# Kernel tuning notes

Hardware: AMD Instinct MI355X
Metric: run time of the kernel (lower is better)

The kernel has to match this reference:

```python
import jax, jax.numpy as jnp
import numpy as np

D_MODEL = 512
N_HEADS = 8
HEAD_DIM = D_MODEL // N_HEADS
SEQ = 2048
BATCH = 2
EPS = 1e-5
SCALE = 1.0 / np.sqrt(HEAD_DIM).astype(np.float32)
# (kind, window, dilation) per head, matching init_kwargs head_specs
SPECS = [("global", 0, 1), ("global", 0, 1),
         ("window", 64, 1), ("window", 128, 1), ("window", 256, 1),
         ("dilated", 64, 2), ("dilated", 64, 4), ("dilated", 64, 8)]


def build_masks(N):
    i = jnp.arange(N)
    D = jnp.abs(i[:, None] - i[None, :])
    ms = []
    for kind, w, dil in SPECS:
        if kind == "global":
            ms.append(jnp.ones((N, N), dtype=bool))
        elif kind == "window":
            ms.append(D <= w)
        else:  # dilated
            ms.append((D % dil == 0) & (D // dil <= w))
    return jnp.stack(ms)  # [H, N, N] bool


def layernorm(x, g, b):
    mu = jnp.mean(x, axis=-1, keepdims=True)
    var = jnp.mean((x - mu) ** 2, axis=-1, keepdims=True)
    return (x - mu) * jax.lax.rsqrt(var + EPS) * g + b


def setup_inputs() -> dict:
    key = jax.random.key(0)
    ks = jax.random.split(key, 7)
    w = 0.02
    return {
        "x": jax.random.normal(ks[0], (BATCH, SEQ, D_MODEL), dtype=jnp.float32),
        "Wq": jax.random.normal(ks[1], (D_MODEL, D_MODEL), dtype=jnp.float32) * w,
        "Wk": jax.random.normal(ks[2], (D_MODEL, D_MODEL), dtype=jnp.float32) * w,
        "Wv": jax.random.normal(ks[3], (D_MODEL, D_MODEL), dtype=jnp.float32) * w,
        "Wo": jax.random.normal(ks[4], (D_MODEL, D_MODEL), dtype=jnp.float32) * w,
        "T_w1": jax.random.normal(ks[5], (D_MODEL, D_MODEL), dtype=jnp.float32) * w,
        "T_b1": jnp.zeros((D_MODEL,), dtype=jnp.float32),
        "T_w2": jax.random.normal(ks[6], (1, D_MODEL), dtype=jnp.float32) * w,
        "T_b2": jnp.zeros((1,), dtype=jnp.float32),
        "ln_in_g": jnp.ones((D_MODEL,), dtype=jnp.float32),
        "ln_in_b": jnp.zeros((D_MODEL,), dtype=jnp.float32),
        "ln_out_g": jnp.ones((D_MODEL,), dtype=jnp.float32),
        "ln_out_b": jnp.zeros((D_MODEL,), dtype=jnp.float32),
    }


def reference(x, Wq, Wk, Wv, Wo, T_w1, T_b1, T_w2, T_b2,
              ln_in_g, ln_in_b, ln_out_g, ln_out_b):
    B, N, H = x.shape
    x0 = x
    xn = layernorm(x, ln_in_g, ln_in_b)
    # torch Linear: y = x @ W.T ; reshape to [B, h, N, d]
    def heads(W):
        return (xn @ W.T).reshape(B, N, N_HEADS, HEAD_DIM).transpose(0, 2, 1, 3)
    Q, K, V = heads(Wq), heads(Wk), heads(Wv)
    attn = jnp.einsum("bhqd,bhkd->bhqk", Q, K) * SCALE
    mask = build_masks(N)  # [h, N, N]
    attn = jnp.where(mask[None], attn, -jnp.inf)
    attn = jax.nn.softmax(attn, axis=-1)  # every row has diagonal unmasked
    out = jnp.einsum("bhqk,bhkd->bhqd", attn, V)
    out = out.transpose(0, 2, 1, 3).reshape(B, N, N_HEADS * HEAD_DIM)
    out = out @ Wo.T
    # tanh-gated softmax over sequence dim
    T_logits = jnp.tanh(xn @ T_w1.T + T_b1) @ T_w2.T + T_b2  # [B, N, 1]
    T = jax.nn.softmax(T_logits, axis=1)
    out = out * T
    return layernorm(out + x0, ln_out_g, ln_out_b)
```

## Files before the change

### kernel.cpp

```cpp
#include <hip/hip_runtime.h>
#include <math.h>

#define N_SEQ 2048
#define DM    512
#define NTOK  4096
#define NH    8
#define HD    64
#define NSLOT 18

typedef __attribute__((ext_vector_type(8))) short short8;
typedef __attribute__((ext_vector_type(4))) short short4_t;
typedef __attribute__((ext_vector_type(4))) float f32x4;

__device__ inline short f2bf(float x) {
    union { float f; unsigned u; } v; v.f = x;
    unsigned r = v.u + 0x7fff + ((v.u >> 16) & 1);
    return (short)(r >> 16);
}
__device__ inline float bf2f(short s) {
    union { unsigned u; float f; } v; v.u = ((unsigned)(unsigned short)s) << 16;
    return v.f;
}
__device__ inline unsigned pkbf(float a, float b) {
    return ((unsigned)(unsigned short)f2bf(b) << 16) | (unsigned)(unsigned short)f2bf(a);
}
__device__ inline float ftanh(float x) {
    float e = __expf(2.f * x);
    return 1.f - 2.f / (e + 1.f);
}

__device__ inline f32x4 mfma16(short8 a, short8 b, f32x4 c) {
    return __builtin_amdgcn_mfma_f32_16x16x32_bf16(a, b, c, 0, 0, 0);
}

__device__ __forceinline__ void async_cp16(const short* g, short* l) {
    __builtin_amdgcn_global_load_lds(
        (const __attribute__((address_space(1))) void*)g,
        (__attribute__((address_space(3))) void*)l, 16, 0, 0);
}

__global__ __launch_bounds__(256) void k_lncvt(
    const float* __restrict__ x, const float* __restrict__ g,
    const float* __restrict__ b, short* __restrict__ y, float* __restrict__ lg,
    const float* __restrict__ Wq, const float* __restrict__ Wk,
    const float* __restrict__ Wv, const float* __restrict__ Tw1,
    const float* __restrict__ Wo,
    short* __restrict__ wcat, short* __restrict__ wo) {
    int blk = blockIdx.x, t = threadIdx.x;
    if (blk < 2048) {
        int sub = t >> 7, tt = t & 127;
        int tk = blk * 2 + sub;
        if (tt == 0) lg[tk] = 0.f;
        float4 xv = ((const float4*)(x + (size_t)tk * DM))[tt];
        float s = xv.x + xv.y + xv.z + xv.w;
        float q = xv.x*xv.x + xv.y*xv.y + xv.z*xv.z + xv.w*xv.w;
        for (int o = 32; o; o >>= 1) { s += __shfl_down(s, o); q += __shfl_down(q, o); }
        __shared__ float ls[4], lq[4];
        if ((t & 63) == 0) { ls[t >> 6] = s; lq[t >> 6] = q; }
        __syncthreads();
        s = ls[sub * 2] + ls[sub * 2 + 1];
        q = lq[sub * 2] + lq[sub * 2 + 1];
        float mu = s * (1.f / DM);
        float var = q * (1.f / DM) - mu * mu;
        float rs = rsqrtf(var + 1e-5f);
        float4 gv = ((const float4*)g)[tt], bv = ((const float4*)b)[tt];
        short4_t o;
        o[0] = f2bf((xv.x - mu) * rs * gv.x + bv.x);
        o[1] = f2bf((xv.y - mu) * rs * gv.y + bv.y);
        o[2] = f2bf((xv.z - mu) * rs * gv.z + bv.z);
        o[3] = f2bf((xv.w - mu) * rs * gv.w + bv.w);
        *(short4_t*)&y[(size_t)tk * DM + tt * 4] = o;
    } else {
        int id = (blk - 2048) * 256 + t;
        if (id < 262144) {
            int z = id >> 16; int off = id & 65535;
            const float* s = (z == 0) ? Wq : (z == 1) ? Wk : (z == 2) ? Wv : Tw1;
            float4 v = ((const float4*)s)[off];
            short4_t o = {f2bf(v.x), f2bf(v.y), f2bf(v.z), f2bf(v.w)};
            *(short4_t*)(wcat + (size_t)z * 262144 + (size_t)off * 4) = o;
        } else {
            int off = id - 262144;
            float4 v = ((const float4*)Wo)[off];
            short4_t o = {f2bf(v.x), f2bf(v.y), f2bf(v.z), f2bf(v.w)};
            *(short4_t*)(wo + (size_t)off * 4) = o;
        }
    }
}

__global__ __launch_bounds__(256) void k_gemmqkvt(
    const short* __restrict__ A, const short* __restrict__ W,
    const float* __restrict__ Tb1, const float* __restrict__ Tw2,
    short* __restrict__ qb, short* __restrict__ kb, short* __restrict__ vb,
    float* __restrict__ lg) {
    __shared__ short As[128 * 32];
    __shared__ short Bs[128 * 32];
    int t = threadIdx.x;
    int lane = t & 63, w = t >> 6;
    int wy = w >> 1, wx = w & 1;
    int ln = lane & 15, q4 = lane >> 4;
    int c0 = blockIdx.x * 128, m0 = blockIdx.y * 128;
    int sr = t >> 2, sc = (t & 3) << 3;
    f32x4 acc[4][4];
    f32x4 zero = {0.f, 0.f, 0.f, 0.f};
    #pragma unroll
    for (int i = 0; i < 4; i++)
        #pragma unroll
        for (int j = 0; j < 4; j++) acc[i][j] = zero;
    for (int k0 = 0; k0 < DM; k0 += 32) {
        __syncthreads();
        async_cp16(&A[(size_t)(m0 + sr) * DM + k0 + sc],      &As[sr * 32 + sc]);
        async_cp16(&A[(size_t)(m0 + 64 + sr) * DM + k0 + sc], &As[(64 + sr) * 32 + sc]);
        async_cp16(&W[(size_t)(c0 + sr) * DM + k0 + sc],      &Bs[sr * 32 + sc]);
        async_cp16(&W[(size_t)(c0 + 64 + sr) * DM + k0 + sc], &Bs[(64 + sr) * 32 + sc]);
        __syncthreads();
        short8 af[4], bfr[4];
        #pragma unroll
        for (int i = 0; i < 4; i++)
            af[i] = *(short8*)&As[(wy * 64 + i * 16 + ln) * 32 + q4 * 8];
        #pragma unroll
        for (int j = 0; j < 4; j++)
            bfr[j] = *(short8*)&Bs[(wx * 64 + j * 16 + ln) * 32 + q4 * 8];
        #pragma unroll
        for (int i = 0; i < 4; i++)
            #pragma unroll
            for (int j = 0; j < 4; j++)
                acc[i][j] = mfma16(af[i], bfr[j], acc[i][j]);
    }
    int z = c0 >> 9;
    if (z < 3) {
        short* dst = (z == 0) ? qb : (z == 1) ? kb : vb;
        float sc2 = (z == 0) ? 0.125f : 1.0f;
        #pragma unroll
        for (int i = 0; i < 4; i++)
            #pragma unroll
            for (int j = 0; j < 4; j++)
                #pragma unroll
                for (int r = 0; r < 4; r++) {
                    int row = m0 + wy * 64 + i * 16 + q4 * 4 + r;
                    int col = c0 + wx * 64 + j * 16 + ln;
                    int nin = col & 511;
                    int h = nin >> 6, d = nin & 63;
                    int bi = row >> 11, n = row & (N_SEQ - 1);
                    dst[(((size_t)bi * NH + h) * N_SEQ + n) * HD + d] =
                        f2bf(acc[i][j][r] * sc2);
                }
    } else {
        #pragma unroll
        for (int i = 0; i < 4; i++) {
            #pragma unroll
            for (int r = 0; r < 4; r++) {
                float s = 0.f;
                #pragma unroll
                for (int j = 0; j < 4; j++) {
                    int tc = (c0 & 511) + wx * 64 + j * 16 + ln;
                    s += ftanh(acc[i][j][r] + Tb1[tc]) * Tw2[tc];
                }
                s += __shfl_xor(s, 1);
                s += __shfl_xor(s, 2);
                s += __shfl_xor(s, 4);
                s += __shfl_xor(s, 8);
                if (ln == 0) {
                    int row = m0 + wy * 64 + i * 16 + q4 * 4 + r;
                    atomicAdd(&lg[row], s);
                }
            }
        }
    }
}

__global__ __launch_bounds__(256) void k_gemmp(
    const short* __restrict__ A, const short* __restrict__ W,
    float* __restrict__ proj) {
    __shared__ short As[128 * 32];
    __shared__ short Bs[64 * 32];
    int t = threadIdx.x;
    int lane = t & 63, w = t >> 6;
    int wy = w >> 1, wx = w & 1;
    int ln = lane & 15, q4 = lane >> 4;
    int c0 = blockIdx.x * 64, m0 = blockIdx.y * 128;
    int sr = t >> 2, sc = (t & 3) << 3;
    int br = t >> 2, bc = (t & 3) << 3;
    f32x4 acc[4][2];
    f32x4 zero = {0.f, 0.f, 0.f, 0.f};
    #pragma unroll
    for (int i = 0; i < 4; i++) { acc[i][0] = zero; acc[i][1] = zero; }
    for (int k0 = 0; k0 < DM; k0 += 32) {
        __syncthreads();
        async_cp16(&A[(size_t)(m0 + sr) * DM + k0 + sc],      &As[sr * 32 + sc]);
        async_cp16(&A[(size_t)(m0 + 64 + sr) * DM + k0 + sc], &As[(64 + sr) * 32 + sc]);
        if (br < 64)
            async_cp16(&W[(size_t)(c0 + br) * DM + k0 + bc], &Bs[br * 32 + bc]);
        __syncthreads();
        short8 af[4], bfr[2];
        #pragma unroll
        for (int i = 0; i < 4; i++)
            af[i] = *(short8*)&As[(wy * 64 + i * 16 + ln) * 32 + q4 * 8];
        #pragma unroll
        for (int j = 0; j < 2; j++)
            bfr[j] = *(short8*)&Bs[(wx * 32 + j * 16 + ln) * 32 + q4 * 8];
        #pragma unroll
        for (int i = 0; i < 4; i++)
            #pragma unroll
            for (int j = 0; j < 2; j++)
                acc[i][j] = mfma16(af[i], bfr[j], acc[i][j]);
    }
    #pragma unroll
    for (int i = 0; i < 4; i++)
        #pragma unroll
        for (int j = 0; j < 2; j++)
            #pragma unroll
            for (int r = 0; r < 4; r++) {
                int row = m0 + wy * 64 + i * 16 + q4 * 4 + r;
                int col = c0 + wx * 32 + j * 16 + ln;
                proj[(size_t)row * DM + col] = acc[i][j][r];
            }
}

__global__ __launch_bounds__(256) void k_vtrgate(const short* __restrict__ vb,
                                                 short* __restrict__ vtb,
                                                 const float* __restrict__ lg,
                                                 float* __restrict__ gate) {
    __shared__ short tile[64][80];
    __shared__ float rg[8];
    int blk = blockIdx.x, t = threadIdx.x;
    if (blk < 512) {
        int n0 = (blk & 31) * 64, bh = blk >> 5;
        const short* src = vb + (size_t)bh * N_SEQ * HD;
        short* dst = vtb + (size_t)bh * HD * N_SEQ;
        #pragma unroll
        for (int i = 0; i < 2; i++) {
            int id = t + 256 * i;
            int r = id >> 3, c = id & 7;
            *(short8*)&tile[r][c * 8] = *(const short8*)&src[(size_t)(n0 + r) * HD + c * 8];
        }
        __syncthreads();
        #pragma unroll
        for (int i = 0; i < 2; i++) {
            int id = t + 256 * i;
            int d = id >> 3, c = id & 7;
            short8 v;
            #pragma unroll
            for (int j = 0; j < 8; j++) v[j] = tile[c * 8 + j][d];
            *(short8*)&dst[(size_t)d * N_SEQ + n0 + c * 8] = v;
        }
    } else {
        int b = blk - 512;
        float v[8];
        {
            float4 a0 = *(const float4*)&lg[b * N_SEQ + t * 8];
            float4 a1 = *(const float4*)&lg[b * N_SEQ + t * 8 + 4];
            v[0] = a0.x; v[1] = a0.y; v[2] = a0.z; v[3] = a0.w;
            v[4] = a1.x; v[5] = a1.y; v[6] = a1.z; v[7] = a1.w;
        }
        float m = v[0];
        #pragma unroll
        for (int j = 1; j < 8; j++) m = fmaxf(m, v[j]);
        for (int o = 32; o; o >>= 1) m = fmaxf(m, __shfl_down(m, o));
        if ((t & 63) == 0) rg[t >> 6] = m;
        __syncthreads();
        m = fmaxf(fmaxf(rg[0], rg[1]), fmaxf(rg[2], rg[3]));
        float e[8], s = 0.f;
        #pragma unroll
        for (int j = 0; j < 8; j++) { e[j] = __expf(v[j] - m); s += e[j]; }
        for (int o = 32; o; o >>= 1) s += __shfl_down(s, o);
        if ((t & 63) == 0) rg[4 + (t >> 6)] = s;
        __syncthreads();
        s = (rg[4] + rg[5]) + (rg[6] + rg[7]);
        float inv = 1.f / s;
        float4 o0 = {e[0] * inv, e[1] * inv, e[2] * inv, e[3] * inv};
        float4 o1 = {e[4] * inv, e[5] * inv, e[6] * inv, e[7] * inv};
        *(float4*)&gate[b * N_SEQ + t * 8] = o0;
        *(float4*)&gate[b * N_SEQ + t * 8 + 4] = o1;
    }
}

__global__ __launch_bounds__(256) void k_attn(const short* __restrict__ qb,
                                              const short* __restrict__ kb,
                                              const short* __restrict__ vtb,
                                              short* __restrict__ P_O,
                                              float* __restrict__ P_ml) {
    __shared__ short Ks[128 * 72];
    __shared__ short Vt[64 * 136];
    __shared__ short Pa[4][16 * 136];
    int t = threadIdx.x;
    int lane = t & 63, w = t >> 6;
    int ln = lane & 15, q4 = lane >> 4;
    int slot = blockIdx.x, qt = blockIdx.y, bi = blockIdx.z;
    int q0 = qt * 64;
    int h, c;
    if (slot < 4)        { h = 0; c = slot; }
    else if (slot < 8)   { h = 1; c = slot - 4; }
    else if (slot == 8)  { h = 2; c = 0; }
    else if (slot == 9)  { h = 3; c = 0; }
    else if (slot < 12)  { h = 4; c = slot - 10; }
    else if (slot == 12) { h = 5; c = 0; }
    else if (slot < 15)  { h = 6; c = slot - 13; }
    else                 { h = 7; c = slot - 15; }
    int kind = (h < 2) ? 0 : (h < 5) ? 1 : 2;
    int wnd = (h == 2 || h >= 5) ? 64 : (h == 3) ? 128 : (h == 4) ? 256 : 0;
    int dsh = (h == 5) ? 1 : (h == 6) ? 2 : (h == 7) ? 3 : 0;
    int dmask = (1 << dsh) - 1;
    int wmax = (kind == 0) ? 0 : (wnd << dsh);
    int tLoU, tHiU, CS;
    if (kind == 0) { tLoU = 0; tHiU = 15; CS = 4; }
    else { tLoU = (q0 - wmax) >> 7; tHiU = (q0 + 63 + wmax) >> 7; CS = 3; }
    int ktLo = tLoU + c * CS;
    int ktHi = ktLo + CS - 1;
    if (ktHi > tHiU) ktHi = tHiU;
    if (ktHi > 15) ktHi = 15;
    if (ktLo < 0) ktLo = 0;
    int p4 = (bi * 32 + qt) * NSLOT + slot;
    float* ml = P_ml + (size_t)p4 * 128;
    if (ktLo > ktHi) {
        if (t < 64) { ml[t] = -1e30f; ml[64 + t] = 0.f; }
        return;
    }
    const size_t base = ((size_t)bi * NH + h) * N_SEQ * HD;
    const short* Q = qb + base;
    const short* K = kb + base;
    const short* Vg = vtb + base;
    short8 qa[2];
    {
        const short* qrow = Q + (size_t)(q0 + w * 16 + ln) * HD + q4 * 8;
        qa[0] = *(const short8*)qrow;
        qa[1] = *(const short8*)(qrow + 32);
    }
    int qi = q0 + w * 16 + ln;
    float m_i = -1e30f, l_i = 0.f;
    f32x4 OT[4];
    f32x4 zero = {0.f, 0.f, 0.f, 0.f};
    #pragma unroll
    for (int d = 0; d < 4; d++) OT[d] = zero;
    short* Paw = Pa[w];
    for (int kt = ktLo; kt <= ktHi; kt++) {
        int k0 = kt << 7;
        __syncthreads();
        #pragma unroll
        for (int i2 = 0; i2 < 4; i2++) {
            int id = t + 256 * i2;
            int kr = id >> 3, cc = id & 7;
            *(short8*)&Ks[kr * 72 + cc * 8] =
                *(const short8*)&K[(size_t)(k0 + kr) * HD + cc * 8];
            int dr = id >> 4, kc = id & 15;
            *(short8*)&Vt[dr * 136 + kc * 8] =
                *(const short8*)&Vg[(size_t)dr * N_SEQ + k0 + kc * 8];
        }
        __syncthreads();
        f32x4 ST[8];
        #pragma unroll
        for (int nt = 0; nt < 8; nt++) ST[nt] = zero;
        #pragma unroll
        for (int nt = 0; nt < 8; nt++) {
            #pragma unroll
            for (int ks = 0; ks < 2; ks++) {
                short8 af = *(short8*)&Ks[(nt * 16 + ln) * 72 + ks * 32 + q4 * 8];
                ST[nt] = mfma16(af, qa[ks], ST[nt]);
            }
        }
        if (kind != 0) {
            #pragma unroll
            for (int nt = 0; nt < 8; nt++)
                #pragma unroll
                for (int r = 0; r < 4; r++) {
                    int key = k0 + nt * 16 + q4 * 4 + r;
                    int dlt = qi - key; dlt = (dlt < 0) ? -dlt : dlt;
                    int valid;
                    if (kind == 1) valid = (dlt <= wnd);
                    else valid = ((dlt & dmask) == 0) && ((dlt >> dsh) <= wnd);
                    if (!valid) ST[nt][r] = -1e30f;
                }
        }
        float rm = -1e30f;
        #pragma unroll
        for (int nt = 0; nt < 8; nt++) {
            float a = fmaxf(ST[nt][0], ST[nt][1]);
            float b = fmaxf(ST[nt][2], ST[nt][3]);
            rm = fmaxf(rm, fmaxf(a, b));
        }
        rm = fmaxf(rm, __shfl_xor(rm, 16));
        rm = fmaxf(rm, __shfl_xor(rm, 32));
        float mn = fmaxf(m_i, rm);
        float sc = __expf(m_i - mn);
        float rs = 0.f;
        #pragma unroll
        for (int nt = 0; nt < 8; nt++) {
            float p0 = __expf(ST[nt][0] - mn);
            float p1 = __expf(ST[nt][1] - mn);
            float p2 = __expf(ST[nt][2] - mn);
            float p3 = __expf(ST[nt][3] - mn);
            rs += (p0 + p1) + (p2 + p3);
            *(unsigned*)&Paw[ln * 136 + nt * 16 + q4 * 4]     = pkbf(p0, p1);
            *(unsigned*)&Paw[ln * 136 + nt * 16 + q4 * 4 + 2] = pkbf(p2, p3);
        }
        rs += __shfl_xor(rs, 16);
        rs += __shfl_xor(rs, 32);
        l_i = l_i * sc + rs;
        m_i = mn;
        #pragma unroll
        for (int d = 0; d < 4; d++) OT[d] *= sc;
        short8 pb[4];
        #pragma unroll
        for (int ks = 0; ks < 4; ks++)
            pb[ks] = *(short8*)&Paw[ln * 136 + ks * 32 + q4 * 8];
        #pragma unroll
        for (int dt = 0; dt < 4; dt++) {
            #pragma unroll
            for (int ks = 0; ks < 4; ks++) {
                short8 a = *(short8*)&Vt[(dt * 16 + ln) * 136 + ks * 32 + q4 * 8];
                OT[dt] = mfma16(a, pb[ks], OT[dt]);
            }
        }
    }
    if (q4 == 0) { ml[w * 16 + ln] = m_i; ml[64 + w * 16 + ln] = l_i; }
    #pragma unroll
    for (int dt = 0; dt < 4; dt++) {
        *(unsigned*)&Paw[ln * 136 + dt * 16 + q4 * 4]     = pkbf(OT[dt][0], OT[dt][1]);
        *(unsigned*)&Paw[ln * 136 + dt * 16 + q4 * 4 + 2] = pkbf(OT[dt][2], OT[dt][3]);
    }
    short8 o0 = *(short8*)&Paw[ln * 136 + q4 * 16];
    short8 o1 = *(short8*)&Paw[ln * 136 + q4 * 16 + 8];
    short* Op = P_O + (size_t)p4 * 4096;
    *(short8*)&Op[(w * 16 + ln) * 64 + q4 * 16] = o0;
    *(short8*)&Op[(w * 16 + ln) * 64 + q4 * 16 + 8] = o1;
}

__global__ __launch_bounds__(256) void k_combine(const short* __restrict__ P_O,
                                                 const float* __restrict__ P_ml,
                                                 short* __restrict__ ob) {
    const int hbase[8] = {0, 4, 8, 9, 10, 12, 13, 15};
    const int hcnt[8]  = {4, 4, 1, 1, 2, 1, 2, 3};
    int h = blockIdx.x, qt = blockIdx.y, bi = blockIdx.z;
    int t = threadIdx.x;
    int row = t >> 2, c0 = (t & 3) * 16;
    int pb = (bi * 32 + qt) * NSLOT + hbase[h];
    int cnt = hcnt[h];
    float m = -1e30f;
    for (int s = 0; s < cnt; s++)
        m = fmaxf(m, P_ml[(size_t)(pb + s) * 128 + row]);
    float l = 0.f;
    float acc[16];
    #pragma unroll
    for (int j = 0; j < 16; j++) acc[j] = 0.f;
    for (int s = 0; s < cnt; s++) {
        float ms = P_ml[(size_t)(pb + s) * 128 + row];
        float ls = P_ml[(size_t)(pb + s) * 128 + 64 + row];
        if (ls > 0.f) {
            float sc = __expf(ms - m);
            l += ls * sc;
            const short* Op = P_O + (size_t)(pb + s) * 4096 + row * 64 + c0;
            short8 v0 = *(const short8*)Op;
            short8 v1 = *(const short8*)(Op + 8);
            #pragma unroll
            for (int j = 0; j < 8; j++) acc[j]     += bf2f(v0[j]) * sc;
            #pragma unroll
            for (int j = 0; j < 8; j++) acc[8 + j] += bf2f(v1[j]) * sc;
        }
    }
    float inv = 1.f / l;
    int n = qt * 64 + row;
    short8 o0, o1;
    #pragma unroll
    for (int j = 0; j < 8; j++) o0[j] = f2bf(acc[j] * inv);
    #pragma unroll
    for (int j = 0; j < 8; j++) o1[j] = f2bf(acc[8 + j] * inv);
    short* dst = ob + ((size_t)bi * N_SEQ + n) * DM + h * 64 + c0;
    *(short8*)dst = o0;
    *(short8*)(dst + 8) = o1;
}

__global__ __launch_bounds__(128) void k_final(const float* __restrict__ proj,
                                               const float* __restrict__ gate,
                                               const float* __restrict__ x0,
                                               const float* __restrict__ g,
                                               const float* __restrict__ b,
                                               float* __restrict__ out) {
    int tk = blockIdx.x, t = threadIdx.x;
    float gt = gate[tk];
    float4 pv = ((const float4*)(proj + (size_t)tk * DM))[t];
    float4 xv = ((const float4*)(x0 + (size_t)tk * DM))[t];
    float4 y;
    y.x = pv.x * gt + xv.x;
    y.y = pv.y * gt + xv.y;
    y.z = pv.z * gt + xv.z;
    y.w = pv.w * gt + xv.w;
    float s = y.x + y.y + y.z + y.w;
    float q = y.x*y.x + y.y*y.y + y.z*y.z + y.w*y.w;
    for (int o = 32; o; o >>= 1) { s += __shfl_down(s, o); q += __shfl_down(q, o); }
    __shared__ float ls[2], lq[2];
    if ((t & 63) == 0) { ls[t >> 6] = s; lq[t >> 6] = q; }
    __syncthreads();
    s = ls[0] + ls[1]; q = lq[0] + lq[1];
    float mu = s * (1.f / DM);
    float var = q * (1.f / DM) - mu * mu;
    float rs = rsqrtf(var + 1e-5f);
    float4 gv = ((const float4*)g)[t], bv = ((const float4*)b)[t];
    float4 o;
    o.x = (y.x - mu) * rs * gv.x + bv.x;
    o.y = (y.y - mu) * rs * gv.y + bv.y;
    o.z = (y.z - mu) * rs * gv.z + bv.z;
    o.w = (y.w - mu) * rs * gv.w + bv.w;
    ((float4*)(out + (size_t)tk * DM))[t] = o;
}

extern "C" void kernel_launch(void* const* d_in, const int* in_sizes, int n_in,
                              void* d_out, int out_size, void* d_ws, size_t ws_size,
                              hipStream_t stream) {
    (void)in_sizes; (void)n_in; (void)out_size; (void)ws_size;
    const float* x    = (const float*)d_in[0];
    const float* Wq   = (const float*)d_in[1];
    const float* Wk   = (const float*)d_in[2];
    const float* Wv   = (const float*)d_in[3];
    const float* Wo   = (const float*)d_in[4];
    const float* Tw1  = (const float*)d_in[5];
    const float* Tb1  = (const float*)d_in[6];
    const float* Tw2  = (const float*)d_in[7];
    const float* ling = (const float*)d_in[9];
    const float* linb = (const float*)d_in[10];
    const float* logg = (const float*)d_in[11];
    const float* logb = (const float*)d_in[12];
    float* out = (float*)d_out;

    const size_t SZ = (size_t)NTOK * DM;
    const int NPART = 2 * 32 * NSLOT;
    char* p = (char*)d_ws;
    short* xn   = (short*)p; p += SZ * 2;
    short* wcat = (short*)p; p += (size_t)2048 * DM * 2;
    short* wo   = (short*)p; p += (size_t)DM * DM * 2;
    short* qb   = (short*)p; p += SZ * 2;
    short* kb   = (short*)p; p += SZ * 2;
    short* vb   = (short*)p; p += SZ * 2;
    short* vtb  = (short*)p; p += SZ * 2;
    short* obuf = (short*)p; p += SZ * 2;
    float* lg   = (float*)p; p += (size_t)NTOK * 4;
    float* gate = (float*)p; p += (size_t)NTOK * 4;
    float* P_ml = (float*)p; p += (size_t)NPART * 128 * 4;
    float* proj = (float*)p;
    short* P_O  = (short*)p; p += (size_t)NPART * 4096 * 2;

    k_lncvt<<<3328, 256, 0, stream>>>(x, ling, linb, xn, lg,
                                      Wq, Wk, Wv, Tw1, Wo, wcat, wo);
    k_gemmqkvt<<<dim3(16, 32), 256, 0, stream>>>(xn, wcat, Tb1, Tw2,
                                                 qb, kb, vb, lg);
    k_vtrgate<<<514, 256, 0, stream>>>(vb, vtb, lg, gate);
    k_attn<<<dim3(NSLOT, 32, 2), 256, 0, stream>>>(qb, kb, vtb, P_O, P_ml);
    k_combine<<<dim3(8, 32, 2), 256, 0, stream>>>(P_O, P_ml, obuf);
    k_gemmp<<<dim3(8, 32), 256, 0, stream>>>(obuf, wo, proj);
    k_final<<<NTOK, 128, 0, stream>>>(proj, gate, x, logg, logb, out);
}
```

Baseline: 162.6 us.

## Fuse V transpose into QKV GEMM and gate softmax into attention kernel

The QKV GEMM epilogue now writes V directly in transposed layout through a shared-memory staging tile, so the separate transpose/gate kernel and the intermediate V buffer are removed. The gate softmax over the sequence moves into one attention block per batch. Single-slot heads (slots 8, 9, 12) normalize their output and write it straight to the output buffer, so the combine kernel handles only the five multi-slot heads. This saves one kernel launch and some global traffic, at the cost of extra shared memory in the GEMM (lower occupancy) and a serial gate tail in one attention block.

```diff
diff --git a/kernel.cpp b/kernel.cpp
--- a/kernel.cpp
+++ b/kernel.cpp
@@ -90,10 +90,11 @@
 __global__ __launch_bounds__(256) void k_gemmqkvt(
     const short* __restrict__ A, const short* __restrict__ W,
     const float* __restrict__ Tb1, const float* __restrict__ Tw2,
-    short* __restrict__ qb, short* __restrict__ kb, short* __restrict__ vb,
+    short* __restrict__ qb, short* __restrict__ kb, short* __restrict__ vtb,
     float* __restrict__ lg) {
     __shared__ short As[128 * 32];
     __shared__ short Bs[128 * 32];
+    __shared__ short Vs[128 * 136];
     int t = threadIdx.x;
     int lane = t & 63, w = t >> 6;
     int wy = w >> 1, wx = w & 1;
@@ -127,8 +128,8 @@
                 acc[i][j] = mfma16(af[i], bfr[j], acc[i][j]);
     }
     int z = c0 >> 9;
-    if (z < 3) {
-        short* dst = (z == 0) ? qb : (z == 1) ? kb : vb;
+    if (z < 2) {
+        short* dst = (z == 0) ? qb : kb;
         float sc2 = (z == 0) ? 0.125f : 1.0f;
         #pragma unroll
         for (int i = 0; i < 4; i++)
@@ -144,6 +145,28 @@
                     dst[(((size_t)bi * NH + h) * N_SEQ + n) * HD + d] =
                         f2bf(acc[i][j][r] * sc2);
                 }
+    } else if (z == 2) {
+        #pragma unroll
+        for (int i = 0; i < 4; i++)
+            #pragma unroll
+            for (int j = 0; j < 4; j++)
+                #pragma unroll
+                for (int r = 0; r < 4; r++) {
+                    int nl = wy * 64 + i * 16 + q4 * 4 + r;
+                    int dl = wx * 64 + j * 16 + ln;
+                    Vs[dl * 136 + nl] = f2bf(acc[i][j][r]);
+                }
+        __syncthreads();
+        int bi = m0 >> 11, n0 = m0 & (N_SEQ - 1);
+        int hp = (c0 & 511) >> 6;
+        #pragma unroll
+        for (int ii = 0; ii < 8; ii++) {
+            int id = t + 256 * ii;
+            int dl = id >> 4, nc = id & 15;
+            short8 v = *(short8*)&Vs[dl * 136 + nc * 8];
+            int h = hp + (dl >> 6), d = dl & 63;
+            *(short8*)&vtb[(((size_t)bi * NH + h) * HD + d) * N_SEQ + n0 + nc * 8] = v;
+        }
     } else {
         #pragma unroll
         for (int i = 0; i < 4; i++) {
@@ -216,72 +239,18 @@
             }
 }
 
-__global__ __launch_bounds__(256) void k_vtrgate(const short* __restrict__ vb,
-                                                 short* __restrict__ vtb,
-                                                 const float* __restrict__ lg,
-                                                 float* __restrict__ gate) {
-    __shared__ short tile[64][80];
-    __shared__ float rg[8];
-    int blk = blockIdx.x, t = threadIdx.x;
-    if (blk < 512) {
-        int n0 = (blk & 31) * 64, bh = blk >> 5;
-        const short* src = vb + (size_t)bh * N_SEQ * HD;
-        short* dst = vtb + (size_t)bh * HD * N_SEQ;
-        #pragma unroll
-        for (int i = 0; i < 2; i++) {
-            int id = t + 256 * i;
-            int r = id >> 3, c = id & 7;
-            *(short8*)&tile[r][c * 8] = *(const short8*)&src[(size_t)(n0 + r) * HD + c * 8];
-        }
-        __syncthreads();
-        #pragma unroll
-        for (int i = 0; i < 2; i++) {
-            int id = t + 256 * i;
-            int d = id >> 3, c = id & 7;
-            short8 v;
-            #pragma unroll
-            for (int j = 0; j < 8; j++) v[j] = tile[c * 8 + j][d];
-            *(short8*)&dst[(size_t)d * N_SEQ + n0 + c * 8] = v;
-        }
-    } else {
-        int b = blk - 512;
-        float v[8];
-        {
-            float4 a0 = *(const float4*)&lg[b * N_SEQ + t * 8];
-            float4 a1 = *(const float4*)&lg[b * N_SEQ + t * 8 + 4];
-            v[0] = a0.x; v[1] = a0.y; v[2] = a0.z; v[3] = a0.w;
-            v[4] = a1.x; v[5] = a1.y; v[6] = a1.z; v[7] = a1.w;
-        }
-        float m = v[0];
-        #pragma unroll
-        for (int j = 1; j < 8; j++) m = fmaxf(m, v[j]);
-        for (int o = 32; o; o >>= 1) m = fmaxf(m, __shfl_down(m, o));
-        if ((t & 63) == 0) rg[t >> 6] = m;
-        __syncthreads();
-        m = fmaxf(fmaxf(rg[0], rg[1]), fmaxf(rg[2], rg[3]));
-        float e[8], s = 0.f;
-        #pragma unroll
-        for (int j = 0; j < 8; j++) { e[j] = __expf(v[j] - m); s += e[j]; }
-        for (int o = 32; o; o >>= 1) s += __shfl_down(s, o);
-        if ((t & 63) == 0) rg[4 + (t >> 6)] = s;
-        __syncthreads();
-        s = (rg[4] + rg[5]) + (rg[6] + rg[7]);
-        float inv = 1.f / s;
-        float4 o0 = {e[0] * inv, e[1] * inv, e[2] * inv, e[3] * inv};
-        float4 o1 = {e[4] * inv, e[5] * inv, e[6] * inv, e[7] * inv};
-        *(float4*)&gate[b * N_SEQ + t * 8] = o0;
-        *(float4*)&gate[b * N_SEQ + t * 8 + 4] = o1;
-    }
-}
-
 __global__ __launch_bounds__(256) void k_attn(const short* __restrict__ qb,
                                               const short* __restrict__ kb,
                                               const short* __restrict__ vtb,
                                               short* __restrict__ P_O,
-                                              float* __restrict__ P_ml) {
+                                              float* __restrict__ P_ml,
+                                              short* __restrict__ ob,
+                                              const float* __restrict__ lg,
+                                              float* __restrict__ gate) {
     __shared__ short Ks[128 * 72];
     __shared__ short Vt[64 * 136];
     __shared__ short Pa[4][16 * 136];
+    __shared__ float rg[8];
     int t = threadIdx.x;
     int lane = t & 63, w = t >> 6;
     int ln = lane & 15, q4 = lane >> 4;
@@ -296,6 +265,7 @@
     else if (slot == 12) { h = 5; c = 0; }
     else if (slot < 15)  { h = 6; c = slot - 13; }
     else                 { h = 7; c = slot - 15; }
+    int solo = (slot == 8) | (slot == 9) | (slot == 12);
     int kind = (h < 2) ? 0 : (h < 5) ? 1 : 2;
     int wnd = (h == 2 || h >= 5) ? 64 : (h == 3) ? 128 : (h == 4) ? 256 : 0;
     int dsh = (h == 5) ? 1 : (h == 6) ? 2 : (h == 7) ? 3 : 0;
@@ -411,29 +381,72 @@
             }
         }
     }
-    if (q4 == 0) { ml[w * 16 + ln] = m_i; ml[64 + w * 16 + ln] = l_i; }
-    #pragma unroll
-    for (int dt = 0; dt < 4; dt++) {
-        *(unsigned*)&Paw[ln * 136 + dt * 16 + q4 * 4]     = pkbf(OT[dt][0], OT[dt][1]);
-        *(unsigned*)&Paw[ln * 136 + dt * 16 + q4 * 4 + 2] = pkbf(OT[dt][2], OT[dt][3]);
-    }
-    short8 o0 = *(short8*)&Paw[ln * 136 + q4 * 16];
-    short8 o1 = *(short8*)&Paw[ln * 136 + q4 * 16 + 8];
-    short* Op = P_O + (size_t)p4 * 4096;
-    *(short8*)&Op[(w * 16 + ln) * 64 + q4 * 16] = o0;
-    *(short8*)&Op[(w * 16 + ln) * 64 + q4 * 16 + 8] = o1;
+    if (solo) {
+        float inv = 1.f / l_i;
+        #pragma unroll
+        for (int dt = 0; dt < 4; dt++) {
+            *(unsigned*)&Paw[ln * 136 + dt * 16 + q4 * 4]     = pkbf(OT[dt][0] * inv, OT[dt][1] * inv);
+            *(unsigned*)&Paw[ln * 136 + dt * 16 + q4 * 4 + 2] = pkbf(OT[dt][2] * inv, OT[dt][3] * inv);
+        }
+        short8 o0 = *(short8*)&Paw[ln * 136 + q4 * 16];
+        short8 o1 = *(short8*)&Paw[ln * 136 + q4 * 16 + 8];
+        short* dst = ob + ((size_t)bi * N_SEQ + q0 + w * 16 + ln) * DM + h * 64 + q4 * 16;
+        *(short8*)dst = o0;
+        *(short8*)(dst + 8) = o1;
+    } else {
+        if (q4 == 0) { ml[w * 16 + ln] = m_i; ml[64 + w * 16 + ln] = l_i; }
+        #pragma unroll
+        for (int dt = 0; dt < 4; dt++) {
+            *(unsigned*)&Paw[ln * 136 + dt * 16 + q4 * 4]     = pkbf(OT[dt][0], OT[dt][1]);
+            *(unsigned*)&Paw[ln * 136 + dt * 16 + q4 * 4 + 2] = pkbf(OT[dt][2], OT[dt][3]);
+        }
+        short8 o0 = *(short8*)&Paw[ln * 136 + q4 * 16];
+        short8 o1 = *(short8*)&Paw[ln * 136 + q4 * 16 + 8];
+        short* Op = P_O + (size_t)p4 * 4096;
+        *(short8*)&Op[(w * 16 + ln) * 64 + q4 * 16] = o0;
+        *(short8*)&Op[(w * 16 + ln) * 64 + q4 * 16 + 8] = o1;
+    }
+    if (slot == 8 && qt == 0) {
+        int b = bi;
+        float v[8];
+        float4 a0 = *(const float4*)&lg[b * N_SEQ + t * 8];
+        float4 a1 = *(const float4*)&lg[b * N_SEQ + t * 8 + 4];
+        v[0] = a0.x; v[1] = a0.y; v[2] = a0.z; v[3] = a0.w;
+        v[4] = a1.x; v[5] = a1.y; v[6] = a1.z; v[7] = a1.w;
+        float m = v[0];
+        #pragma unroll
+        for (int j = 1; j < 8; j++) m = fmaxf(m, v[j]);
+        for (int o = 32; o; o >>= 1) m = fmaxf(m, __shfl_down(m, o));
+        if ((t & 63) == 0) rg[t >> 6] = m;
+        __syncthreads();
+        m = fmaxf(fmaxf(rg[0], rg[1]), fmaxf(rg[2], rg[3]));
+        float e[8], s = 0.f;
+        #pragma unroll
+        for (int j = 0; j < 8; j++) { e[j] = __expf(v[j] - m); s += e[j]; }
+        for (int o = 32; o; o >>= 1) s += __shfl_down(s, o);
+        if ((t & 63) == 0) rg[4 + (t >> 6)] = s;
+        __syncthreads();
+        s = (rg[4] + rg[5]) + (rg[6] + rg[7]);
+        float inv = 1.f / s;
+        float4 o0 = {e[0] * inv, e[1] * inv, e[2] * inv, e[3] * inv};
+        float4 o1 = {e[4] * inv, e[5] * inv, e[6] * inv, e[7] * inv};
+        *(float4*)&gate[b * N_SEQ + t * 8] = o0;
+        *(float4*)&gate[b * N_SEQ + t * 8 + 4] = o1;
+    }
 }
 
 __global__ __launch_bounds__(256) void k_combine(const short* __restrict__ P_O,
                                                  const float* __restrict__ P_ml,
                                                  short* __restrict__ ob) {
-    const int hbase[8] = {0, 4, 8, 9, 10, 12, 13, 15};
-    const int hcnt[8]  = {4, 4, 1, 1, 2, 1, 2, 3};
-    int h = blockIdx.x, qt = blockIdx.y, bi = blockIdx.z;
+    const int hsel[5]  = {0, 1, 4, 6, 7};
+    const int hbase[5] = {0, 4, 10, 13, 15};
+    const int hcnt[5]  = {4, 4, 2, 2, 3};
+    int hh = blockIdx.x, qt = blockIdx.y, bi = blockIdx.z;
+    int h = hsel[hh];
     int t = threadIdx.x;
     int row = t >> 2, c0 = (t & 3) * 16;
-    int pb = (bi * 32 + qt) * NSLOT + hbase[h];
-    int cnt = hcnt[h];
+    int pb = (bi * 32 + qt) * NSLOT + hbase[hh];
+    int cnt = hcnt[hh];
     float m = -1e30f;
     for (int s = 0; s < cnt; s++)
         m = fmaxf(m, P_ml[(size_t)(pb + s) * 128 + row]);
@@ -528,7 +541,6 @@
     short* wo   = (short*)p; p += (size_t)DM * DM * 2;
     short* qb   = (short*)p; p += SZ * 2;
     short* kb   = (short*)p; p += SZ * 2;
-    short* vb   = (short*)p; p += SZ * 2;
     short* vtb  = (short*)p; p += SZ * 2;
     short* obuf = (short*)p; p += SZ * 2;
     float* lg   = (float*)p; p += (size_t)NTOK * 4;
@@ -540,10 +552,10 @@
     k_lncvt<<<3328, 256, 0, stream>>>(x, ling, linb, xn, lg,
                                       Wq, Wk, Wv, Tw1, Wo, wcat, wo);
     k_gemmqkvt<<<dim3(16, 32), 256, 0, stream>>>(xn, wcat, Tb1, Tw2,
-                                                 qb, kb, vb, lg);
-    k_vtrgate<<<514, 256, 0, stream>>>(vb, vtb, lg, gate);
-    k_attn<<<dim3(NSLOT, 32, 2), 256, 0, stream>>>(qb, kb, vtb, P_O, P_ml);
-    k_combine<<<dim3(8, 32, 2), 256, 0, stream>>>(P_O, P_ml, obuf);
+                                                 qb, kb, vtb, lg);
+    k_attn<<<dim3(NSLOT, 32, 2), 256, 0, stream>>>(qb, kb, vtb, P_O, P_ml,
+                                                   obuf, lg, gate);
+    k_combine<<<dim3(5, 32, 2), 256, 0, stream>>>(P_O, P_ml, obuf);
     k_gemmp<<<dim3(8, 32), 256, 0, stream>>>(obuf, wo, proj);
     k_final<<<NTOK, 128, 0, stream>>>(proj, gate, x, logg, logb, out);
 }
```

Measured after the change: 159.0 us. 1.02x faster.
